# Kernel optimization log

Hardware: AMD Instinct MI355X
Metric: run time of the kernel (lower is better)

The kernel has to match this reference:

```python
import jax, jax.numpy as jnp
import numpy as np

N_NODES = 50000
N_EDGES = 600000
IN_FEATS, HID_FEATS, OUT_FEATS = 128, 128, 64


def setup_inputs() -> dict:
    key = jax.random.key(0)
    ks = jax.random.split(key, 6)
    x = jax.random.normal(ks[0], (N_NODES, IN_FEATS), dtype=jnp.float32)
    src = jax.random.randint(ks[1], (N_EDGES,), 0, N_NODES, dtype=jnp.int32)
    dst = jax.random.randint(ks[2], (N_EDGES,), 0, N_NODES, dtype=jnp.int32)
    # Xavier-ish init for the two fc_neigh linear layers
    W1 = jax.random.normal(ks[3], (IN_FEATS, HID_FEATS), dtype=jnp.float32) * (1.0 / np.sqrt(IN_FEATS))
    b1 = jnp.zeros((HID_FEATS,), dtype=jnp.float32)
    W2 = jax.random.normal(ks[4], (HID_FEATS, OUT_FEATS), dtype=jnp.float32) * (1.0 / np.sqrt(HID_FEATS))
    b2 = jnp.zeros((OUT_FEATS,), dtype=jnp.float32)
    return {"x": x, "src": src, "dst": dst, "W1": W1, "b1": b1, "W2": W2, "b2": b2}


def _sage_gcn_layer(h, src, dst, W, b, deg):
    # DGL SAGEConv(aggregator_type='gcn'):
    #   h_neigh[i] = (sum_{j in in-nbrs(i)} h[j] + h[i]) / (in_deg[i] + 1)
    #   out = h_neigh @ W + b   (no separate fc_self for 'gcn')
    msg_sum = jax.ops.segment_sum(h[src], dst, num_segments=N_NODES)  # [N, d]
    h_neigh = (msg_sum + h) / (deg + 1.0)[:, None]
    return h_neigh @ W + b


def reference(x, src, dst, W1, b1, W2, b2):
    # in-degree per destination node (shared by both layers)
    deg = jax.ops.segment_sum(jnp.ones_like(dst, dtype=x.dtype), dst, num_segments=N_NODES)  # [N]
    h = _sage_gcn_layer(x, src, dst, W1, b1, deg)
    h = jax.nn.relu(h)
    h = _sage_gcn_layer(h, src, dst, W2, b2, deg)
    return h
```

## Files before the change

### kernel.cpp

```cpp
#include <hip/hip_runtime.h>

#define NF 128

typedef __attribute__((ext_vector_type(8))) short short8;
typedef __attribute__((ext_vector_type(4))) float f32x4;

__device__ inline ushort f2bf(float f) {
    uint u = __float_as_uint(f);
    return (ushort)((u + 0x7FFFu + ((u >> 16) & 1u)) >> 16);
}
__device__ inline float bf2f(ushort u) {
    return __uint_as_float(((uint)u) << 16);
}

__global__ __launch_bounds__(256) void prep_kernel(
    const float* __restrict__ x, const float* __restrict__ W1,
    const float* __restrict__ W2, int* __restrict__ cnt,
    ushort* __restrict__ xb, ushort* __restrict__ W1t, ushort* __restrict__ W2t,
    int n_nodes, int n8) {
    int gid = blockIdx.x * 256 + threadIdx.x;
    int gstride = gridDim.x * 256;
    for (int i = gid; i < n_nodes; i += gstride) cnt[i] = 0;
    for (int i = gid; i < 128 * 128; i += gstride) {
        int k = i >> 7, n = i & 127;
        W1t[n * NF + k] = f2bf(W1[i]);
    }
    for (int i = gid; i < 128 * 64; i += gstride) {
        int k = i >> 6, n = i & 63;
        W2t[n * NF + k] = f2bf(W2[i]);
    }
    const float4* in4 = reinterpret_cast<const float4*>(x);
    for (int i = gid; i < n8; i += gstride) {
        float4 v0 = in4[i * 2], v1 = in4[i * 2 + 1];
        short8 o;
        o[0] = (short)f2bf(v0.x); o[1] = (short)f2bf(v0.y);
        o[2] = (short)f2bf(v0.z); o[3] = (short)f2bf(v0.w);
        o[4] = (short)f2bf(v1.x); o[5] = (short)f2bf(v1.y);
        o[6] = (short)f2bf(v1.z); o[7] = (short)f2bf(v1.w);
        *reinterpret_cast<short8*>(&xb[i * 8]) = o;
    }
}

__global__ void hist_kernel(const int* __restrict__ dst, int* __restrict__ cnt,
                            int n_edges) {
    int i = blockIdx.x * blockDim.x + threadIdx.x;
    if (i < n_edges) atomicAdd(&cnt[dst[i]], 1);
}

__global__ __launch_bounds__(256) void reduce_kernel(const int* __restrict__ cnt,
                                                     int* __restrict__ partials,
                                                     int n) {
    __shared__ int s[256];
    int t = threadIdx.x;
    int i = blockIdx.x * 256 + t;
    s[t] = (i < n) ? cnt[i] : 0;
    __syncthreads();
    for (int off = 128; off > 0; off >>= 1) {
        if (t < off) s[t] += s[t + off];
        __syncthreads();
    }
    if (t == 0) partials[blockIdx.x] = s[0];
}

__global__ __launch_bounds__(256) void scan_apply_kernel(int* __restrict__ cnt,
                                                         int* __restrict__ rowptr,
                                                         const int* __restrict__ partials,
                                                         int n) {
    __shared__ int s[256];
    __shared__ int off0_sh;
    int t = threadIdx.x;
    s[t] = (t < (int)blockIdx.x) ? partials[t] : 0;
    __syncthreads();
    for (int off = 128; off > 0; off >>= 1) {
        if (t < off) s[t] += s[t + off];
        __syncthreads();
    }
    if (t == 0) off0_sh = s[0];
    __syncthreads();
    int off0 = off0_sh;
    __syncthreads();
    int i = blockIdx.x * 256 + t;
    int v = (i < n) ? cnt[i] : 0;
    s[t] = v;
    __syncthreads();
    for (int off = 1; off < 256; off <<= 1) {
        int a = (t >= off) ? s[t - off] : 0;
        __syncthreads();
        s[t] += a;
        __syncthreads();
    }
    if (i < n) {
        rowptr[i + 1] = off0 + s[t];
        cnt[i] = off0 + s[t] - v;
    }
    if (blockIdx.x == 0 && t == 0) rowptr[0] = 0;
}

__global__ void fill_kernel(const int* __restrict__ src,
                            const int* __restrict__ dst,
                            int* __restrict__ cursor,
                            int* __restrict__ edge_src, int n_edges) {
    int i = blockIdx.x * blockDim.x + threadIdx.x;
    if (i < n_edges) {
        int slot = atomicAdd(&cursor[dst[i]], 1);
        edge_src[slot] = src[i];
    }
}

__global__ __launch_bounds__(256) void aggregate_kernel(
    const ushort* __restrict__ hb, const int* __restrict__ rowptr,
    const int* __restrict__ edge_src, ushort* __restrict__ hn, int n_nodes) {
    int t = threadIdx.x;
    int g = t & 31;
    int node = blockIdx.x * 8 + (t >> 5);
    if (node >= n_nodes) return;
    const ushort4* h4 = reinterpret_cast<const ushort4*>(hb);
    int e0 = rowptr[node], e1 = rowptr[node + 1];
    ushort4 sv = h4[(size_t)node * 32 + g];
    float a0x = bf2f(sv.x), a0y = bf2f(sv.y), a0z = bf2f(sv.z), a0w = bf2f(sv.w);
    float a1x = 0.f, a1y = 0.f, a1z = 0.f, a1w = 0.f;
    float a2x = 0.f, a2y = 0.f, a2z = 0.f, a2w = 0.f;
    float a3x = 0.f, a3y = 0.f, a3z = 0.f, a3w = 0.f;
    for (int base = e0; base < e1; base += 32) {
        int m = min(32, e1 - base);
        int sg = (base + g < e1) ? edge_src[base + g] : 0;
        int j = 0;
        for (; j + 4 <= m; j += 4) {
            int s0 = __shfl(sg, j, 32);
            int s1 = __shfl(sg, j + 1, 32);
            int s2 = __shfl(sg, j + 2, 32);
            int s3 = __shfl(sg, j + 3, 32);
            ushort4 v0 = h4[(size_t)s0 * 32 + g];
            ushort4 v1 = h4[(size_t)s1 * 32 + g];
            ushort4 v2 = h4[(size_t)s2 * 32 + g];
            ushort4 v3 = h4[(size_t)s3 * 32 + g];
            a0x += bf2f(v0.x); a0y += bf2f(v0.y); a0z += bf2f(v0.z); a0w += bf2f(v0.w);
            a1x += bf2f(v1.x); a1y += bf2f(v1.y); a1z += bf2f(v1.z); a1w += bf2f(v1.w);
            a2x += bf2f(v2.x); a2y += bf2f(v2.y); a2z += bf2f(v2.z); a2w += bf2f(v2.w);
            a3x += bf2f(v3.x); a3y += bf2f(v3.y); a3z += bf2f(v3.z); a3w += bf2f(v3.w);
        }
        for (; j < m; ++j) {
            int s = __shfl(sg, j, 32);
            ushort4 v = h4[(size_t)s * 32 + g];
            a0x += bf2f(v.x); a0y += bf2f(v.y); a0z += bf2f(v.z); a0w += bf2f(v.w);
        }
    }
    float inv = 1.0f / (float)(e1 - e0 + 1);
    ushort4 o;
    o.x = f2bf((a0x + a1x + a2x + a3x) * inv);
    o.y = f2bf((a0y + a1y + a2y + a3y) * inv);
    o.z = f2bf((a0z + a1z + a2z + a3z) * inv);
    o.w = f2bf((a0w + a1w + a2w + a3w) * inv);
    reinterpret_cast<ushort4*>(hn)[(size_t)node * 32 + g] = o;
}

__global__ __launch_bounds__(256) void aggregate64_kernel(
    const ushort* __restrict__ y, const int* __restrict__ rowptr,
    const int* __restrict__ edge_src, const float* __restrict__ b,
    float* __restrict__ out, int n_nodes) {
    int t = threadIdx.x;
    int g = t & 15;
    int node = blockIdx.x * 16 + (t >> 4);
    if (node >= n_nodes) return;
    const ushort4* y4 = reinterpret_cast<const ushort4*>(y);
    int e0 = rowptr[node], e1 = rowptr[node + 1];
    ushort4 sv = y4[(size_t)node * 16 + g];
    float a0x = bf2f(sv.x), a0y = bf2f(sv.y), a0z = bf2f(sv.z), a0w = bf2f(sv.w);
    float a1x = 0.f, a1y = 0.f, a1z = 0.f, a1w = 0.f;
    float a2x = 0.f, a2y = 0.f, a2z = 0.f, a2w = 0.f;
    float a3x = 0.f, a3y = 0.f, a3z = 0.f, a3w = 0.f;
    for (int base = e0; base < e1; base += 16) {
        int m = min(16, e1 - base);
        int sg = (base + g < e1) ? edge_src[base + g] : 0;
        int j = 0;
        for (; j + 4 <= m; j += 4) {
            int s0 = __shfl(sg, j, 16);
            int s1 = __shfl(sg, j + 1, 16);
            int s2 = __shfl(sg, j + 2, 16);
            int s3 = __shfl(sg, j + 3, 16);
            ushort4 v0 = y4[(size_t)s0 * 16 + g];
            ushort4 v1 = y4[(size_t)s1 * 16 + g];
            ushort4 v2 = y4[(size_t)s2 * 16 + g];
            ushort4 v3 = y4[(size_t)s3 * 16 + g];
            a0x += bf2f(v0.x); a0y += bf2f(v0.y); a0z += bf2f(v0.z); a0w += bf2f(v0.w);
            a1x += bf2f(v1.x); a1y += bf2f(v1.y); a1z += bf2f(v1.z); a1w += bf2f(v1.w);
            a2x += bf2f(v2.x); a2y += bf2f(v2.y); a2z += bf2f(v2.z); a2w += bf2f(v2.w);
            a3x += bf2f(v3.x); a3y += bf2f(v3.y); a3z += bf2f(v3.z); a3w += bf2f(v3.w);
        }
        for (; j < m; ++j) {
            int s = __shfl(sg, j, 16);
            ushort4 v = y4[(size_t)s * 16 + g];
            a0x += bf2f(v.x); a0y += bf2f(v.y); a0z += bf2f(v.z); a0w += bf2f(v.w);
        }
    }
    float inv = 1.0f / (float)(e1 - e0 + 1);
    float4 bv = reinterpret_cast<const float4*>(b)[g];
    float4 o;
    o.x = (a0x + a1x + a2x + a3x) * inv + bv.x;
    o.y = (a0y + a1y + a2y + a3y) * inv + bv.y;
    o.z = (a0z + a1z + a2z + a3z) * inv + bv.z;
    o.w = (a0w + a1w + a2w + a3w) * inv + bv.w;
    reinterpret_cast<float4*>(out)[(size_t)node * 16 + g] = o;
}

__global__ __launch_bounds__(256) void gemm12_kernel(
    const ushort* __restrict__ A, const ushort* __restrict__ W1t,
    const float* __restrict__ b1, const ushort* __restrict__ W2t,
    ushort* __restrict__ y, int n_nodes) {
    __shared__ ushort As[64][136];
    __shared__ ushort Ws1[128][136];
    __shared__ ushort Ws2[64][136];

    int t = threadIdx.x;
    int row0 = blockIdx.x * 64;
    for (int i = t; i < 64 * 16; i += 256) {
        int r = i >> 4, c = i & 15;
        int gr = row0 + r;
        short8 v = {};
        if (gr < n_nodes)
            v = *reinterpret_cast<const short8*>(&A[(size_t)gr * NF + c * 8]);
        *reinterpret_cast<short8*>(&As[r][c * 8]) = v;
    }
    for (int i = t; i < 128 * 16; i += 256) {
        int r = i >> 4, c = i & 15;
        *reinterpret_cast<short8*>(&Ws1[r][c * 8]) =
            *reinterpret_cast<const short8*>(&W1t[r * NF + c * 8]);
    }
    for (int i = t; i < 64 * 16; i += 256) {
        int r = i >> 4, c = i & 15;
        *reinterpret_cast<short8*>(&Ws2[r][c * 8]) =
            *reinterpret_cast<const short8*>(&W2t[r * NF + c * 8]);
    }
    __syncthreads();

    int w = t >> 6;
    int l = t & 63;
    int m16 = l & 15;
    int g = l >> 4;
    int m0 = w * 16;

    f32x4 acc1[8];
#pragma unroll
    for (int nt = 0; nt < 8; nt++) acc1[nt] = {0.f, 0.f, 0.f, 0.f};
#pragma unroll
    for (int kk = 0; kk < 4; kk++) {
        int k0 = kk * 32 + g * 8;
        short8 a = *reinterpret_cast<const short8*>(&As[m0 + m16][k0]);
#pragma unroll
        for (int nt = 0; nt < 8; nt++) {
            short8 b = *reinterpret_cast<const short8*>(&Ws1[nt * 16 + m16][k0]);
            acc1[nt] = __builtin_amdgcn_mfma_f32_16x16x32_bf16(a, b, acc1[nt], 0, 0, 0);
        }
    }
    __syncthreads();

#pragma unroll
    for (int nt = 0; nt < 8; nt++) {
        int col = nt * 16 + m16;
        float bv = b1[col];
#pragma unroll
        for (int i = 0; i < 4; i++) {
            int r = m0 + g * 4 + i;
            As[r][col] = f2bf(fmaxf(acc1[nt][i] + bv, 0.f));
        }
    }
    __syncthreads();

    f32x4 acc2[4];
#pragma unroll
    for (int nt = 0; nt < 4; nt++) acc2[nt] = {0.f, 0.f, 0.f, 0.f};
#pragma unroll
    for (int kk = 0; kk < 4; kk++) {
        int k0 = kk * 32 + g * 8;
        short8 a = *reinterpret_cast<const short8*>(&As[m0 + m16][k0]);
#pragma unroll
        for (int nt = 0; nt < 4; nt++) {
            short8 b = *reinterpret_cast<const short8*>(&Ws2[nt * 16 + m16][k0]);
            acc2[nt] = __builtin_amdgcn_mfma_f32_16x16x32_bf16(a, b, acc2[nt], 0, 0, 0);
        }
    }

#pragma unroll
    for (int nt = 0; nt < 4; nt++) {
        int col = nt * 16 + m16;
#pragma unroll
        for (int i = 0; i < 4; i++) {
            int gr = row0 + m0 + g * 4 + i;
            if (gr < n_nodes)
                y[(size_t)gr * 64 + col] = f2bf(acc2[nt][i]);
        }
    }
}

extern "C" void kernel_launch(void* const* d_in, const int* in_sizes, int n_in,
                              void* d_out, int out_size, void* d_ws, size_t ws_size,
                              hipStream_t stream) {
    const float* x   = (const float*)d_in[0];
    const int*   src = (const int*)d_in[1];
    const int*   dst = (const int*)d_in[2];
    const float* W1  = (const float*)d_in[3];
    const float* b1  = (const float*)d_in[4];
    const float* W2  = (const float*)d_in[5];
    const float* b2  = (const float*)d_in[6];
    float* out = (float*)d_out;

    int n_nodes = in_sizes[0] / NF;
    int n_edges = in_sizes[1];
    int nb = (n_nodes + 255) / 256;
    int n8 = n_nodes * NF / 8;

    int* rowptr   = (int*)d_ws;
    int* cnt      = rowptr + (n_nodes + 4);
    int* edge_src = cnt + n_nodes;
    int* partials = edge_src + n_edges;
    size_t iw = (size_t)(n_nodes + 4) + n_nodes + n_edges + 256;
    iw = (iw + 63) & ~(size_t)63;
    ushort* W1t = (ushort*)((int*)d_ws + iw);
    ushort* W2t = W1t + 128 * NF;
    ushort* xb  = W2t + 64 * NF;
    ushort* hn  = xb + (size_t)n_nodes * NF;
    ushort* y   = hn + (size_t)n_nodes * NF;

    int eb = (n_edges + 255) / 256;

    prep_kernel<<<1024, 256, 0, stream>>>(x, W1, W2, cnt, xb, W1t, W2t, n_nodes, n8);
    hist_kernel<<<eb, 256, 0, stream>>>(dst, cnt, n_edges);
    reduce_kernel<<<nb, 256, 0, stream>>>(cnt, partials, n_nodes);
    scan_apply_kernel<<<nb, 256, 0, stream>>>(cnt, rowptr, partials, n_nodes);
    fill_kernel<<<eb, 256, 0, stream>>>(src, dst, cnt, edge_src, n_edges);

    int ab = (n_nodes + 7) / 8;
    int gb = (n_nodes + 63) / 64;

    aggregate_kernel<<<ab, 256, 0, stream>>>(xb, rowptr, edge_src, hn, n_nodes);
    gemm12_kernel<<<gb, 256, 0, stream>>>(hn, W1t, b1, W2t, y, n_nodes);
    aggregate64_kernel<<<(n_nodes + 15) / 16, 256, 0, stream>>>(y, rowptr, edge_src, b2, out, n_nodes);
}
```

Measured before the change: 131.5 us.

## Widen aggregation gathers to 16-byte loads, merge scan kernels, read W2 from global

```diff
diff --git a/kernel.cpp b/kernel.cpp
--- a/kernel.cpp
+++ b/kernel.cpp
@@ -47,39 +47,26 @@
     if (i < n_edges) atomicAdd(&cnt[dst[i]], 1);
 }
 
-__global__ __launch_bounds__(256) void reduce_kernel(const int* __restrict__ cnt,
-                                                     int* __restrict__ partials,
-                                                     int n) {
+__global__ __launch_bounds__(256) void scan_apply_kernel(
+    const int* __restrict__ cnt, int* __restrict__ rowptr,
+    int* __restrict__ cursor, int n) {
     __shared__ int s[256];
+    __shared__ int off0_sh;
     int t = threadIdx.x;
-    int i = blockIdx.x * 256 + t;
-    s[t] = (i < n) ? cnt[i] : 0;
+    int lim = (int)blockIdx.x * 256;
+    int sum = 0;
+    for (int i = t; i < lim; i += 256) sum += cnt[i];
+    s[t] = sum;
     __syncthreads();
     for (int off = 128; off > 0; off >>= 1) {
         if (t < off) s[t] += s[t + off];
         __syncthreads();
     }
-    if (t == 0) partials[blockIdx.x] = s[0];
-}
-
-__global__ __launch_bounds__(256) void scan_apply_kernel(int* __restrict__ cnt,
-                                                         int* __restrict__ rowptr,
-                                                         const int* __restrict__ partials,
-                                                         int n) {
-    __shared__ int s[256];
-    __shared__ int off0_sh;
-    int t = threadIdx.x;
-    s[t] = (t < (int)blockIdx.x) ? partials[t] : 0;
-    __syncthreads();
-    for (int off = 128; off > 0; off >>= 1) {
-        if (t < off) s[t] += s[t + off];
-        __syncthreads();
-    }
     if (t == 0) off0_sh = s[0];
     __syncthreads();
     int off0 = off0_sh;
     __syncthreads();
-    int i = blockIdx.x * 256 + t;
+    int i = lim + t;
     int v = (i < n) ? cnt[i] : 0;
     s[t] = v;
     __syncthreads();
@@ -91,7 +78,7 @@
     }
     if (i < n) {
         rowptr[i + 1] = off0 + s[t];
-        cnt[i] = off0 + s[t] - v;
+        cursor[i] = off0 + s[t] - v;
     }
     if (blockIdx.x == 0 && t == 0) rowptr[0] = 0;
 }
@@ -111,64 +98,20 @@
     const ushort* __restrict__ hb, const int* __restrict__ rowptr,
     const int* __restrict__ edge_src, ushort* __restrict__ hn, int n_nodes) {
     int t = threadIdx.x;
-    int g = t & 31;
-    int node = blockIdx.x * 8 + (t >> 5);
-    if (node >= n_nodes) return;
-    const ushort4* h4 = reinterpret_cast<const ushort4*>(hb);
-    int e0 = rowptr[node], e1 = rowptr[node + 1];
-    ushort4 sv = h4[(size_t)node * 32 + g];
-    float a0x = bf2f(sv.x), a0y = bf2f(sv.y), a0z = bf2f(sv.z), a0w = bf2f(sv.w);
-    float a1x = 0.f, a1y = 0.f, a1z = 0.f, a1w = 0.f;
-    float a2x = 0.f, a2y = 0.f, a2z = 0.f, a2w = 0.f;
-    float a3x = 0.f, a3y = 0.f, a3z = 0.f, a3w = 0.f;
-    for (int base = e0; base < e1; base += 32) {
-        int m = min(32, e1 - base);
-        int sg = (base + g < e1) ? edge_src[base + g] : 0;
-        int j = 0;
-        for (; j + 4 <= m; j += 4) {
-            int s0 = __shfl(sg, j, 32);
-            int s1 = __shfl(sg, j + 1, 32);
-            int s2 = __shfl(sg, j + 2, 32);
-            int s3 = __shfl(sg, j + 3, 32);
-            ushort4 v0 = h4[(size_t)s0 * 32 + g];
-            ushort4 v1 = h4[(size_t)s1 * 32 + g];
-            ushort4 v2 = h4[(size_t)s2 * 32 + g];
-            ushort4 v3 = h4[(size_t)s3 * 32 + g];
-            a0x += bf2f(v0.x); a0y += bf2f(v0.y); a0z += bf2f(v0.z); a0w += bf2f(v0.w);
-            a1x += bf2f(v1.x); a1y += bf2f(v1.y); a1z += bf2f(v1.z); a1w += bf2f(v1.w);
-            a2x += bf2f(v2.x); a2y += bf2f(v2.y); a2z += bf2f(v2.z); a2w += bf2f(v2.w);
-            a3x += bf2f(v3.x); a3y += bf2f(v3.y); a3z += bf2f(v3.z); a3w += bf2f(v3.w);
-        }
-        for (; j < m; ++j) {
-            int s = __shfl(sg, j, 32);
-            ushort4 v = h4[(size_t)s * 32 + g];
-            a0x += bf2f(v.x); a0y += bf2f(v.y); a0z += bf2f(v.z); a0w += bf2f(v.w);
-        }
-    }
-    float inv = 1.0f / (float)(e1 - e0 + 1);
-    ushort4 o;
-    o.x = f2bf((a0x + a1x + a2x + a3x) * inv);
-    o.y = f2bf((a0y + a1y + a2y + a3y) * inv);
-    o.z = f2bf((a0z + a1z + a2z + a3z) * inv);
-    o.w = f2bf((a0w + a1w + a2w + a3w) * inv);
-    reinterpret_cast<ushort4*>(hn)[(size_t)node * 32 + g] = o;
-}
-
-__global__ __launch_bounds__(256) void aggregate64_kernel(
-    const ushort* __restrict__ y, const int* __restrict__ rowptr,
-    const int* __restrict__ edge_src, const float* __restrict__ b,
-    float* __restrict__ out, int n_nodes) {
-    int t = threadIdx.x;
     int g = t & 15;
     int node = blockIdx.x * 16 + (t >> 4);
     if (node >= n_nodes) return;
-    const ushort4* y4 = reinterpret_cast<const ushort4*>(y);
+    const short8* h8 = reinterpret_cast<const short8*>(hb);
     int e0 = rowptr[node], e1 = rowptr[node + 1];
-    ushort4 sv = y4[(size_t)node * 16 + g];
-    float a0x = bf2f(sv.x), a0y = bf2f(sv.y), a0z = bf2f(sv.z), a0w = bf2f(sv.w);
-    float a1x = 0.f, a1y = 0.f, a1z = 0.f, a1w = 0.f;
-    float a2x = 0.f, a2y = 0.f, a2z = 0.f, a2w = 0.f;
-    float a3x = 0.f, a3y = 0.f, a3z = 0.f, a3w = 0.f;
+    float a0[8], a1[8], a2[8], a3[8];
+    {
+        short8 sv = h8[(size_t)node * 16 + g];
+#pragma unroll
+        for (int i = 0; i < 8; i++) {
+            a0[i] = bf2f((ushort)sv[i]);
+            a1[i] = 0.f; a2[i] = 0.f; a3[i] = 0.f;
+        }
+    }
     for (int base = e0; base < e1; base += 16) {
         int m = min(16, e1 - base);
         int sg = (base + g < e1) ? edge_src[base + g] : 0;
@@ -178,29 +121,95 @@
             int s1 = __shfl(sg, j + 1, 16);
             int s2 = __shfl(sg, j + 2, 16);
             int s3 = __shfl(sg, j + 3, 16);
-            ushort4 v0 = y4[(size_t)s0 * 16 + g];
-            ushort4 v1 = y4[(size_t)s1 * 16 + g];
-            ushort4 v2 = y4[(size_t)s2 * 16 + g];
-            ushort4 v3 = y4[(size_t)s3 * 16 + g];
-            a0x += bf2f(v0.x); a0y += bf2f(v0.y); a0z += bf2f(v0.z); a0w += bf2f(v0.w);
-            a1x += bf2f(v1.x); a1y += bf2f(v1.y); a1z += bf2f(v1.z); a1w += bf2f(v1.w);
-            a2x += bf2f(v2.x); a2y += bf2f(v2.y); a2z += bf2f(v2.z); a2w += bf2f(v2.w);
-            a3x += bf2f(v3.x); a3y += bf2f(v3.y); a3z += bf2f(v3.z); a3w += bf2f(v3.w);
+            short8 v0 = h8[(size_t)s0 * 16 + g];
+            short8 v1 = h8[(size_t)s1 * 16 + g];
+            short8 v2 = h8[(size_t)s2 * 16 + g];
+            short8 v3 = h8[(size_t)s3 * 16 + g];
+#pragma unroll
+            for (int i = 0; i < 8; i++) {
+                a0[i] += bf2f((ushort)v0[i]);
+                a1[i] += bf2f((ushort)v1[i]);
+                a2[i] += bf2f((ushort)v2[i]);
+                a3[i] += bf2f((ushort)v3[i]);
+            }
         }
         for (; j < m; ++j) {
             int s = __shfl(sg, j, 16);
-            ushort4 v = y4[(size_t)s * 16 + g];
-            a0x += bf2f(v.x); a0y += bf2f(v.y); a0z += bf2f(v.z); a0w += bf2f(v.w);
+            short8 v = h8[(size_t)s * 16 + g];
+#pragma unroll
+            for (int i = 0; i < 8; i++) a0[i] += bf2f((ushort)v[i]);
         }
     }
     float inv = 1.0f / (float)(e1 - e0 + 1);
-    float4 bv = reinterpret_cast<const float4*>(b)[g];
-    float4 o;
-    o.x = (a0x + a1x + a2x + a3x) * inv + bv.x;
-    o.y = (a0y + a1y + a2y + a3y) * inv + bv.y;
-    o.z = (a0z + a1z + a2z + a3z) * inv + bv.z;
-    o.w = (a0w + a1w + a2w + a3w) * inv + bv.w;
-    reinterpret_cast<float4*>(out)[(size_t)node * 16 + g] = o;
+    short8 o;
+#pragma unroll
+    for (int i = 0; i < 8; i++)
+        o[i] = (short)f2bf((a0[i] + a1[i] + a2[i] + a3[i]) * inv);
+    reinterpret_cast<short8*>(hn)[(size_t)node * 16 + g] = o;
+}
+
+__global__ __launch_bounds__(256) void aggregate64_kernel(
+    const ushort* __restrict__ y, const int* __restrict__ rowptr,
+    const int* __restrict__ edge_src, const float* __restrict__ b,
+    float* __restrict__ out, int n_nodes) {
+    int t = threadIdx.x;
+    int g = t & 7;
+    int node = blockIdx.x * 32 + (t >> 3);
+    if (node >= n_nodes) return;
+    const short8* y8 = reinterpret_cast<const short8*>(y);
+    int e0 = rowptr[node], e1 = rowptr[node + 1];
+    float a0[8], a1[8], a2[8], a3[8];
+    {
+        short8 sv = y8[(size_t)node * 8 + g];
+#pragma unroll
+        for (int i = 0; i < 8; i++) {
+            a0[i] = bf2f((ushort)sv[i]);
+            a1[i] = 0.f; a2[i] = 0.f; a3[i] = 0.f;
+        }
+    }
+    for (int base = e0; base < e1; base += 8) {
+        int m = min(8, e1 - base);
+        int sg = (base + g < e1) ? edge_src[base + g] : 0;
+        int j = 0;
+        for (; j + 4 <= m; j += 4) {
+            int s0 = __shfl(sg, j, 8);
+            int s1 = __shfl(sg, j + 1, 8);
+            int s2 = __shfl(sg, j + 2, 8);
+            int s3 = __shfl(sg, j + 3, 8);
+            short8 v0 = y8[(size_t)s0 * 8 + g];
+            short8 v1 = y8[(size_t)s1 * 8 + g];
+            short8 v2 = y8[(size_t)s2 * 8 + g];
+            short8 v3 = y8[(size_t)s3 * 8 + g];
+#pragma unroll
+            for (int i = 0; i < 8; i++) {
+                a0[i] += bf2f((ushort)v0[i]);
+                a1[i] += bf2f((ushort)v1[i]);
+                a2[i] += bf2f((ushort)v2[i]);
+                a3[i] += bf2f((ushort)v3[i]);
+            }
+        }
+        for (; j < m; ++j) {
+            int s = __shfl(sg, j, 8);
+            short8 v = y8[(size_t)s * 8 + g];
+#pragma unroll
+            for (int i = 0; i < 8; i++) a0[i] += bf2f((ushort)v[i]);
+        }
+    }
+    float inv = 1.0f / (float)(e1 - e0 + 1);
+    const float4* b4 = reinterpret_cast<const float4*>(b);
+    float4 bv0 = b4[g * 2], bv1 = b4[g * 2 + 1];
+    float4 o0, o1;
+    o0.x = (a0[0] + a1[0] + a2[0] + a3[0]) * inv + bv0.x;
+    o0.y = (a0[1] + a1[1] + a2[1] + a3[1]) * inv + bv0.y;
+    o0.z = (a0[2] + a1[2] + a2[2] + a3[2]) * inv + bv0.z;
+    o0.w = (a0[3] + a1[3] + a2[3] + a3[3]) * inv + bv0.w;
+    o1.x = (a0[4] + a1[4] + a2[4] + a3[4]) * inv + bv1.x;
+    o1.y = (a0[5] + a1[5] + a2[5] + a3[5]) * inv + bv1.y;
+    o1.z = (a0[6] + a1[6] + a2[6] + a3[6]) * inv + bv1.z;
+    o1.w = (a0[7] + a1[7] + a2[7] + a3[7]) * inv + bv1.w;
+    float4* outp = reinterpret_cast<float4*>(out + (size_t)node * 64 + g * 8);
+    outp[0] = o0;
+    outp[1] = o1;
 }
 
 __global__ __launch_bounds__(256) void gemm12_kernel(
@@ -209,7 +218,6 @@
     ushort* __restrict__ y, int n_nodes) {
     __shared__ ushort As[64][136];
     __shared__ ushort Ws1[128][136];
-    __shared__ ushort Ws2[64][136];
 
     int t = threadIdx.x;
     int row0 = blockIdx.x * 64;
@@ -226,11 +234,6 @@
         *reinterpret_cast<short8*>(&Ws1[r][c * 8]) =
             *reinterpret_cast<const short8*>(&W1t[r * NF + c * 8]);
     }
-    for (int i = t; i < 64 * 16; i += 256) {
-        int r = i >> 4, c = i & 15;
-        *reinterpret_cast<short8*>(&Ws2[r][c * 8]) =
-            *reinterpret_cast<const short8*>(&W2t[r * NF + c * 8]);
-    }
     __syncthreads();
 
     int w = t >> 6;
@@ -275,7 +278,8 @@
         short8 a = *reinterpret_cast<const short8*>(&As[m0 + m16][k0]);
 #pragma unroll
         for (int nt = 0; nt < 4; nt++) {
-            short8 b = *reinterpret_cast<const short8*>(&Ws2[nt * 16 + m16][k0]);
+            short8 b = *reinterpret_cast<const short8*>(
+                &W2t[(size_t)(nt * 16 + m16) * NF + k0]);
             acc2[nt] = __builtin_amdgcn_mfma_f32_16x16x32_bf16(a, b, acc2[nt], 0, 0, 0);
         }
     }
@@ -311,9 +315,9 @@
 
     int* rowptr   = (int*)d_ws;
     int* cnt      = rowptr + (n_nodes + 4);
-    int* edge_src = cnt + n_nodes;
-    int* partials = edge_src + n_edges;
-    size_t iw = (size_t)(n_nodes + 4) + n_nodes + n_edges + 256;
+    int* cursor   = cnt + n_nodes;
+    int* edge_src = cursor + n_nodes;
+    size_t iw = (size_t)(n_nodes + 4) + n_nodes + n_nodes + n_edges;
     iw = (iw + 63) & ~(size_t)63;
     ushort* W1t = (ushort*)((int*)d_ws + iw);
     ushort* W2t = W1t + 128 * NF;
@@ -325,14 +329,10 @@
 
     prep_kernel<<<1024, 256, 0, stream>>>(x, W1, W2, cnt, xb, W1t, W2t, n_nodes, n8);
     hist_kernel<<<eb, 256, 0, stream>>>(dst, cnt, n_edges);
-    reduce_kernel<<<nb, 256, 0, stream>>>(cnt, partials, n_nodes);
-    scan_apply_kernel<<<nb, 256, 0, stream>>>(cnt, rowptr, partials, n_nodes);
-    fill_kernel<<<eb, 256, 0, stream>>>(src, dst, cnt, edge_src, n_edges);
-
-    int ab = (n_nodes + 7) / 8;
-    int gb = (n_nodes + 63) / 64;
-
-    aggregate_kernel<<<ab, 256, 0, stream>>>(xb, rowptr, edge_src, hn, n_nodes);
-    gemm12_kernel<<<gb, 256, 0, stream>>>(hn, W1t, b1, W2t, y, n_nodes);
-    aggregate64_kernel<<<(n_nodes + 15) / 16, 256, 0, stream>>>(y, rowptr, edge_src, b2, out, n_nodes);
-}
+    scan_apply_kernel<<<nb, 256, 0, stream>>>(cnt, rowptr, cursor, n_nodes);
+    fill_kernel<<<eb, 256, 0, stream>>>(src, dst, cursor, edge_src, n_edges);
+
+    aggregate_kernel<<<(n_nodes + 15) / 16, 256, 0, stream>>>(xb, rowptr, edge_src, hn, n_nodes);
+    gemm12_kernel<<<(n_nodes + 63) / 64, 256, 0, stream>>>(hn, W1t, b1, W2t, y, n_nodes);
+    aggregate64_kernel<<<(n_nodes + 31) / 32, 256, 0, stream>>>(y, rowptr, edge_src, b2, out, n_nodes);
+}
```

Result: slower. 155.8 us (+18.5%).
